# Kernel tuning notes

Hardware: AMD Instinct MI355X
Metric: run time of the kernel (lower is better)

The kernel has to match this reference:

```python
import jax, jax.numpy as jnp
import numpy as np

NUM_HEADS = 12
HEAD_DIM = 64
HIDDEN = NUM_HEADS * HEAD_DIM  # 768
B, L = 4, 512

def setup_inputs() -> dict:
    key = jax.random.key(0)
    ks = jax.random.split(key, 8)
    s = 0.02
    return {
        "hidden_states": jax.random.normal(ks[0], (B, L, HIDDEN), jnp.float32),
        "relation_embedding_k": jax.random.normal(ks[1], (B, L, L, HEAD_DIM), jnp.float32),
        "relation_embedding_v": jax.random.normal(ks[2], (B, L, L, HEAD_DIM), jnp.float32),
        "Wq": jax.random.normal(ks[3], (HIDDEN, HIDDEN), jnp.float32) * s,
        "bq": jnp.zeros((HIDDEN,), jnp.float32),
        "Wk": jax.random.normal(ks[4], (HIDDEN, HIDDEN), jnp.float32) * s,
        "bk": jnp.zeros((HIDDEN,), jnp.float32),
        "Wv": jax.random.normal(ks[5], (HIDDEN, HIDDEN), jnp.float32) * s,
        "bv": jnp.zeros((HIDDEN,), jnp.float32),
    }

def _heads(x):
    # [B, L, HIDDEN] -> [B, H, L, D]
    b, l, _ = x.shape
    return x.reshape(b, l, NUM_HEADS, HEAD_DIM).transpose(0, 2, 1, 3)

def reference(hidden_states, relation_embedding_k, relation_embedding_v,
              Wq, bq, Wk, bk, Wv, bv):
    q = _heads(hidden_states @ Wq + bq)  # [B,H,L,D]
    k = _heads(hidden_states @ Wk + bk)
    v = _heads(hidden_states @ Wv + bv)

    # content scores + relation key scores (shared across heads)
    scores = jnp.einsum('bhld,bhmd->bhlm', q, k)
    scores = scores + jnp.einsum('bhld,blrd->bhlr', q, relation_embedding_k)
    scores = scores / np.sqrt(HEAD_DIM).astype(np.float32)

    probs = jax.nn.softmax(scores, axis=-1)  # [B,H,L,L]

    ctx = jnp.einsum('bhlm,bhmd->bhld', probs, v)
    ctx = ctx + jnp.einsum('bhlr,brld->bhld', probs, relation_embedding_v)

    # [B,H,L,D] -> [B,L,HIDDEN]
    b, h, l, d = ctx.shape
    return ctx.transpose(0, 2, 1, 3).reshape(b, l, h * d)
```

## Files before the change

kernel.cpp:

```cpp
#include <hip/hip_runtime.h>
#include <stdint.h>


typedef __attribute__((ext_vector_type(8))) short bf16x8;
typedef __attribute__((ext_vector_type(4))) float f32x4;
typedef __attribute__((ext_vector_type(4))) unsigned int u32x4;

__device__ __forceinline__ unsigned short f2bf(float f) {
  union { float f; unsigned int u; } v; v.f = f;
  unsigned int r = v.u + 0x7fffu + ((v.u >> 16) & 1u);
  return (unsigned short)(r >> 16);
}
__device__ __forceinline__ float bf2f(unsigned short s) {
  union { unsigned int u; float f; } v; v.u = ((unsigned int)s) << 16;
  return v.f;
}
__device__ __forceinline__ void lds_barrier() {
  asm volatile("s_waitcnt lgkmcnt(0)\ns_barrier" ::: "memory");
}

__global__ void k_cvt_hidden(const float* __restrict__ x, unsigned short* __restrict__ y) {
  int i = blockIdx.x * 256 + threadIdx.x;
  float4 v = reinterpret_cast<const float4*>(x)[i];
  ushort4 o;
  o.x = f2bf(v.x); o.y = f2bf(v.y); o.z = f2bf(v.z); o.w = f2bf(v.w);
  reinterpret_cast<ushort4*>(y)[i] = o;
}

__global__ void k_transp_w(const float* __restrict__ Wq, const float* __restrict__ Wk,
                           const float* __restrict__ Wv, unsigned short* __restrict__ wt) {
  __shared__ float t[64][65];
  const int kt = blockIdx.x, nt = blockIdx.y, wsel = blockIdx.z;
  const float* W = wsel == 0 ? Wq : (wsel == 1 ? Wk : Wv);
  const int lx = threadIdx.x & 63, ly = threadIdx.x >> 6;
  for (int i = 0; i < 64; i += 4)
    t[ly + i][lx] = W[(size_t)(kt * 64 + ly + i) * 768 + nt * 64 + lx];
  __syncthreads();
  for (int i = 0; i < 64; i += 4) {
    int r = ly + i;
    wt[((size_t)wsel * 768 + nt * 64 + r) * 768 + kt * 64 + lx] = f2bf(t[lx][r]);
  }
}

__global__ __launch_bounds__(256) void k_qkv_gemm(
    const unsigned short* __restrict__ A, const unsigned short* __restrict__ Bt,
    const float* __restrict__ bq, const float* __restrict__ bk, const float* __restrict__ bv,
    unsigned short* __restrict__ qbf, unsigned short* __restrict__ kbf,
    unsigned short* __restrict__ vbt) {
  __shared__ __align__(16) unsigned short lA[64 * 64];
  __shared__ __align__(16) unsigned short lB[64 * 64];
  const int tid = threadIdx.x, lane = tid & 63, w = tid >> 6;
  const int m0 = blockIdx.x * 64, n0 = blockIdx.y * 64;
  const int wm = (w >> 1) * 32, wn = (w & 1) * 32;
  f32x4 acc[2][2] = {};

  for (int kt = 0; kt < 12; ++kt) {
    __syncthreads();
#pragma unroll
    for (int i = 0; i < 2; ++i) {
      int e16 = i * 256 + tid;
      int row = e16 >> 3;
      int kb = (e16 & 7) * 16;
      int dst = row * 128 + (kb ^ ((row & 7) << 4));
      u32x4 va = *(const u32x4*)((const char*)A + (size_t)(m0 + row) * 1536 + kt * 128 + kb);
      *(u32x4*)((char*)lA + dst) = va;
      u32x4 vb = *(const u32x4*)((const char*)Bt + (size_t)(n0 + row) * 1536 + kt * 128 + kb);
      *(u32x4*)((char*)lB + dst) = vb;
    }
    __syncthreads();
#pragma unroll
    for (int ks = 0; ks < 2; ++ks) {
      bf16x8 fa[2], fb[2];
      const int kbyte = (ks * 32 + (lane >> 4) * 8) * 2;
#pragma unroll
      for (int mi = 0; mi < 2; ++mi) {
        int row = wm + mi * 16 + (lane & 15);
        fa[mi] = *(const bf16x8*)((const char*)lA + row * 128 + (kbyte ^ ((row & 7) << 4)));
      }
#pragma unroll
      for (int ni = 0; ni < 2; ++ni) {
        int row = wn + ni * 16 + (lane & 15);
        fb[ni] = *(const bf16x8*)((const char*)lB + row * 128 + (kbyte ^ ((row & 7) << 4)));
      }
#pragma unroll
      for (int mi = 0; mi < 2; ++mi)
#pragma unroll
        for (int ni = 0; ni < 2; ++ni)
          acc[mi][ni] = __builtin_amdgcn_mfma_f32_16x16x32_bf16(fa[mi], fb[ni], acc[mi][ni], 0, 0, 0);
    }
  }
#pragma unroll
  for (int mi = 0; mi < 2; ++mi)
#pragma unroll
    for (int ni = 0; ni < 2; ++ni) {
      int gn = n0 + wn + ni * 16 + (lane & 15);
      float bias = (gn < 768) ? bq[gn] : (gn < 1536 ? bk[gn - 768] : bv[gn - 1536]);
#pragma unroll
      for (int r = 0; r < 4; ++r) {
        int gm = m0 + wm + mi * 16 + ((lane >> 4) << 2) + r;
        float val = acc[mi][ni][r] + bias;
        int b = gm >> 9, l = gm & 511;
        int d = gn & 63;
        if (gn < 768) {
          int h = gn >> 6;
          qbf[(((size_t)(b * 12 + h)) * 512 + l) * 64 + d] = f2bf(val);
        } else if (gn < 1536) {
          int h = (gn - 768) >> 6;
          kbf[(((size_t)(b * 12 + h)) * 512 + l) * 64 + d] = f2bf(val);
        } else {
          int h = (gn - 1536) >> 6;
          vbt[(((size_t)(b * 12 + h)) * 64 + d) * 512 + l] = f2bf(val);
        }
      }
    }
}

__global__ __launch_bounds__(256) void k_scores(
    const unsigned short* __restrict__ qbf, const unsigned short* __restrict__ kbf,
    float* __restrict__ S) {
  __shared__ __align__(16) unsigned short lQ[64 * 64];
  __shared__ __align__(16) unsigned short lK[64 * 64];
  const int tid = threadIdx.x, lane = tid & 63, w = tid >> 6;
  const int mt = blockIdx.x, lt = blockIdx.y, bh = blockIdx.z;
  const int wm = (w >> 1) * 32, wn = (w & 1) * 32;
  f32x4 acc[2][2] = {};
#pragma unroll
  for (int i = 0; i < 2; ++i) {
    int e16 = i * 256 + tid;
    int row = e16 >> 3;
    int kb = (e16 & 7) * 16;
    int dst = row * 128 + (kb ^ ((row & 7) << 4));
    u32x4 vq = *(const u32x4*)((const char*)qbf + ((size_t)bh * 512 + lt * 64 + row) * 128 + kb);
    *(u32x4*)((char*)lQ + dst) = vq;
    u32x4 vk = *(const u32x4*)((const char*)kbf + ((size_t)bh * 512 + mt * 64 + row) * 128 + kb);
    *(u32x4*)((char*)lK + dst) = vk;
  }
  __syncthreads();
#pragma unroll
  for (int ks = 0; ks < 2; ++ks) {
    bf16x8 fa[2], fb[2];
    const int kbyte = (ks * 32 + (lane >> 4) * 8) * 2;
#pragma unroll
    for (int mi = 0; mi < 2; ++mi) {
      int row = wm + mi * 16 + (lane & 15);
      fa[mi] = *(const bf16x8*)((const char*)lQ + row * 128 + (kbyte ^ ((row & 7) << 4)));
    }
#pragma unroll
    for (int ni = 0; ni < 2; ++ni) {
      int row = wn + ni * 16 + (lane & 15);
      fb[ni] = *(const bf16x8*)((const char*)lK + row * 128 + (kbyte ^ ((row & 7) << 4)));
    }
#pragma unroll
    for (int mi = 0; mi < 2; ++mi)
#pragma unroll
      for (int ni = 0; ni < 2; ++ni)
        acc[mi][ni] = __builtin_amdgcn_mfma_f32_16x16x32_bf16(fa[mi], fb[ni], acc[mi][ni], 0, 0, 0);
  }
#pragma unroll
  for (int mi = 0; mi < 2; ++mi)
#pragma unroll
    for (int ni = 0; ni < 2; ++ni) {
      int gm = mt * 64 + wn + ni * 16 + (lane & 15);
#pragma unroll
      for (int r = 0; r < 4; ++r) {
        int gl = lt * 64 + wm + mi * 16 + ((lane >> 4) << 2) + r;
        S[(size_t)bh * 262144 + (size_t)gl * 512 + gm] = acc[mi][ni][r];
      }
    }
}

__global__ __launch_bounds__(256) void k_rel(
    const unsigned short* __restrict__ qbf,
    const float* __restrict__ relk,
    const float* __restrict__ relv,
    const float* __restrict__ S,
    unsigned short* __restrict__ pbf,
    float* __restrict__ crel) {
  __shared__ __align__(16) char X[24576];
  const int tid = threadIdx.x, lane = tid & 63, w = tid >> 6;
  const int bl = blockIdx.x, b = bl >> 9, l = bl & 511;
  const int lm = lane & 15, lg = lane >> 4;

  const int hq = lm < 12 ? lm : 11;
  const char* qrow = (const char*)qbf + (((size_t)b * 12 + hq) * 512 + l) * 128;
  const bf16x8 qa0 = *(const bf16x8*)(qrow + lg * 16);
  const bf16x8 qa1 = *(const bf16x8*)(qrow + 64 + lg * 16);

  const char* rkb = (const char*)relk + (size_t)bl * 131072 +
                    (size_t)(w * 128 + lm) * 256 + lg * 32;
  f32x4 ld[3][4];
  f32x4 accA[8];
#pragma unroll
  for (int t = 0; t < 8; ++t) accA[t] = {0.f, 0.f, 0.f, 0.f};

#define LOADT(t, s)                                                  \
  {                                                                  \
    const char* p_ = rkb + (size_t)(t) * 4096;                       \
    ld[s][0] = *(const f32x4*)(p_);                                  \
    ld[s][1] = *(const f32x4*)(p_ + 16);                             \
    ld[s][2] = *(const f32x4*)(p_ + 128);                            \
    ld[s][3] = *(const f32x4*)(p_ + 144);                            \
  }
  LOADT(0, 0)
  LOADT(1, 1)
#pragma unroll
  for (int t = 0; t < 8; ++t) {
    if (t < 6) LOADT(t + 2, (t + 2) % 3)
    union { bf16x8 v; unsigned short u[8]; } fb0, fb1;
    const int s = t % 3;
#pragma unroll
    for (int j = 0; j < 4; ++j) {
      fb0.u[j] = f2bf(ld[s][0][j]);
      fb0.u[4 + j] = f2bf(ld[s][1][j]);
      fb1.u[j] = f2bf(ld[s][2][j]);
      fb1.u[4 + j] = f2bf(ld[s][3][j]);
    }
    accA[t] = __builtin_amdgcn_mfma_f32_16x16x32_bf16(qa0, fb0.v, accA[t], 0, 0, 0);
    accA[t] = __builtin_amdgcn_mfma_f32_16x16x32_bf16(qa1, fb1.v, accA[t], 0, 0, 0);
  }
#undef LOADT

  float sreg[3][8];
#pragma unroll
  for (int hh = 0; hh < 3; ++hh) {
    const float* sp = S + (((size_t)b * 12 + (w * 3 + hh)) * 512 + l) * 512 + lane;
#pragma unroll
    for (int j = 0; j < 8; ++j) sreg[hh][j] = sp[j * 64];
  }

  if (lg < 3) {
#pragma unroll
    for (int t = 0; t < 8; ++t) {
      const int r = w * 128 + t * 16 + lm;
#pragma unroll
      for (int reg = 0; reg < 4; ++reg) {
        const int h = lg * 4 + reg;
        *(float*)(X + h * 2048 + ((r * 4) ^ (lg << 6))) = accA[t][reg];
      }
    }
  }
  lds_barrier();

#pragma unroll
  for (int hh = 0; hh < 3; ++hh) {
    const int h = w * 3 + hh;
    const int sw = ((h >> 2) & 3) << 6;
    const size_t srow = (((size_t)b * 12 + h) * 512 + l) * 512;
    float sv[8];
    float mx = -1e30f;
#pragma unroll
    for (int j = 0; j < 8; ++j) {
      const int r = j * 64 + lane;
      float s = (*(const float*)(X + h * 2048 + ((r * 4) ^ sw)) + sreg[hh][j]) * 0.125f;
      sv[j] = s;
      mx = fmaxf(mx, s);
    }
#pragma unroll
    for (int off = 32; off; off >>= 1) mx = fmaxf(mx, __shfl_xor(mx, off));
    float sm = 0.f;
#pragma unroll
    for (int j = 0; j < 8; ++j) { sv[j] = __expf(sv[j] - mx); sm += sv[j]; }
#pragma unroll
    for (int off = 32; off; off >>= 1) sm += __shfl_xor(sm, off);
    const float inv = 1.f / sm;
#pragma unroll
    for (int j = 0; j < 8; ++j) {
      const int r = j * 64 + lane;
      const float pv = sv[j] * inv;
      *(float*)(X + h * 2048 + ((r * 4) ^ sw)) = pv;
      pbf[srow + r] = f2bf(pv);
    }
  }
  lds_barrier();

  float cacc[12];
#pragma unroll
  for (int h = 0; h < 12; ++h) cacc[h] = 0.f;
  const char* vptr = (const char*)relv + (size_t)b * 67108864 +
                     (size_t)(w * 128) * 131072 + (size_t)l * 256 + lane * 4;
#pragma unroll 2
  for (int rc = 0; rc < 32; ++rc) {
    const float v0 = *(const float*)(vptr);
    const float v1 = *(const float*)(vptr + 131072);
    const float v2 = *(const float*)(vptr + 262144);
    const float v3 = *(const float*)(vptr + 393216);
    vptr += 524288;
    const int r0 = w * 128 + rc * 4;
#pragma unroll
    for (int h = 0; h < 12; ++h) {
      const f32x4 p = *(const f32x4*)(X + h * 2048 + ((r0 * 4) ^ (((h >> 2) & 3) << 6)));
      cacc[h] += p[0] * v0 + p[1] * v1 + p[2] * v2 + p[3] * v3;
    }
  }
  lds_barrier();
  float* red = (float*)X;
#pragma unroll
  for (int h = 0; h < 12; ++h) red[(w * 12 + h) * 64 + lane] = cacc[h];
  lds_barrier();
  for (int i = tid; i < 768; i += 256) {
    const int h = i >> 6, d = i & 63;
    crel[(size_t)bl * 768 + i] =
        red[h * 64 + d] + red[(12 + h) * 64 + d] + red[(24 + h) * 64 + d] + red[(36 + h) * 64 + d];
  }
}

__global__ __launch_bounds__(256) void k_pv(
    const unsigned short* __restrict__ pbf, const unsigned short* __restrict__ vbt,
    const float* __restrict__ crel, float* __restrict__ out) {
  __shared__ __align__(16) unsigned short lP[64 * 64];
  __shared__ __align__(16) unsigned short lV[64 * 64];
  const int tid = threadIdx.x, lane = tid & 63, w = tid >> 6;
  const int lt = blockIdx.x, bh = blockIdx.y;
  const int b = bh / 12, h = bh % 12;
  const int wm = (w >> 1) * 32, wn = (w & 1) * 32;
  f32x4 acc[2][2] = {};
  const char* pbase = (const char*)pbf + ((size_t)bh * 512 + lt * 64) * 1024;
  const char* vbase = (const char*)vbt + (size_t)bh * 64 * 1024;
  for (int kt = 0; kt < 8; ++kt) {
    __syncthreads();
#pragma unroll
    for (int i = 0; i < 2; ++i) {
      int e16 = i * 256 + tid;
      int row = e16 >> 3;
      int kb = (e16 & 7) * 16;
      int dst = row * 128 + (kb ^ ((row & 7) << 4));
      u32x4 vp = *(const u32x4*)(pbase + (size_t)row * 1024 + kt * 128 + kb);
      *(u32x4*)((char*)lP + dst) = vp;
      u32x4 vv = *(const u32x4*)(vbase + (size_t)row * 1024 + kt * 128 + kb);
      *(u32x4*)((char*)lV + dst) = vv;
    }
    __syncthreads();
#pragma unroll
    for (int ks = 0; ks < 2; ++ks) {
      bf16x8 fa[2], fb[2];
      const int kbyte = (ks * 32 + (lane >> 4) * 8) * 2;
#pragma unroll
      for (int mi = 0; mi < 2; ++mi) {
        int row = wm + mi * 16 + (lane & 15);
        fa[mi] = *(const bf16x8*)((const char*)lP + row * 128 + (kbyte ^ ((row & 7) << 4)));
      }
#pragma unroll
      for (int ni = 0; ni < 2; ++ni) {
        int row = wn + ni * 16 + (lane & 15);
        fb[ni] = *(const bf16x8*)((const char*)lV + row * 128 + (kbyte ^ ((row & 7) << 4)));
      }
#pragma unroll
      for (int mi = 0; mi < 2; ++mi)
#pragma unroll
        for (int ni = 0; ni < 2; ++ni)
          acc[mi][ni] = __builtin_amdgcn_mfma_f32_16x16x32_bf16(fa[mi], fb[ni], acc[mi][ni], 0, 0, 0);
    }
  }
#pragma unroll
  for (int mi = 0; mi < 2; ++mi)
#pragma unroll
    for (int ni = 0; ni < 2; ++ni) {
      int gd = wn + ni * 16 + (lane & 15);
#pragma unroll
      for (int r = 0; r < 4; ++r) {
        int gl = lt * 64 + wm + mi * 16 + ((lane >> 4) << 2) + r;
        size_t o = ((size_t)b * 512 + gl) * 768 + h * 64 + gd;
        out[o] = acc[mi][ni][r] + crel[o];
      }
    }
}

extern "C" void kernel_launch(void* const* d_in, const int* in_sizes, int n_in,
                              void* d_out, int out_size, void* d_ws, size_t ws_size,
                              hipStream_t stream) {
  (void)in_sizes; (void)n_in; (void)out_size; (void)ws_size;
  const float* hidden = (const float*)d_in[0];
  const float* relk   = (const float*)d_in[1];
  const float* relv   = (const float*)d_in[2];
  const float* Wq     = (const float*)d_in[3];
  const float* bq     = (const float*)d_in[4];
  const float* Wk     = (const float*)d_in[5];
  const float* bk     = (const float*)d_in[6];
  const float* Wv     = (const float*)d_in[7];
  const float* bv     = (const float*)d_in[8];
  float* out = (float*)d_out;
  char* ws = (char*)d_ws;

  unsigned short* hb  = (unsigned short*)(ws);
  unsigned short* wt  = (unsigned short*)(ws + 3145728);
  unsigned short* qbf = (unsigned short*)(ws + 6684672);
  unsigned short* kbf = (unsigned short*)(ws + 9830400);
  unsigned short* vbt = (unsigned short*)(ws + 12976128);
  float*          S   = (float*)(ws + 16121856);
  unsigned short* pbf = (unsigned short*)(ws + 66453504);
  float*          cr  = (float*)(ws + 91619328);

  k_cvt_hidden<<<1536, 256, 0, stream>>>(hidden, hb);
  k_transp_w<<<dim3(12, 12, 3), 256, 0, stream>>>(Wq, Wk, Wv, wt);
  k_qkv_gemm<<<dim3(32, 36), 256, 0, stream>>>(hb, wt, bq, bk, bv, qbf, kbf, vbt);
  k_scores<<<dim3(8, 8, 48), 256, 0, stream>>>(qbf, kbf, S);
  k_rel<<<2048, 256, 0, stream>>>(qbf, relk, relv, S, pbf, cr);
  k_pv<<<dim3(8, 48), 256, 0, stream>>>(pbf, vbt, cr, out);
}
```

Before: 198.8 us.

## Software-pipeline relation-embedding loads in k_rel with inline asm and explicit vmcnt waits

Rewrites the memory-bound k_rel kernel so its global loads are issued through inline asm with explicit s_waitcnt vmcnt. The relk tiles and the relv rows are prefetched into triple-buffered registers, with eight relv rows per stage instead of four. The S loads are issued before the relk pipeline so they overlap, and fp32-to-bf16 conversion uses the packed v_cvt_pk_bf16_f32 instruction. The bf16 probability store is deferred until after the relv accumulation, which keeps the critical path free. This costs more live registers and uses hand-scheduled waits that depend on the exact count of outstanding loads.

```diff
diff --git a/kernel.cpp b/kernel.cpp
--- a/kernel.cpp
+++ b/kernel.cpp
@@ -18,6 +18,23 @@
 __device__ __forceinline__ void lds_barrier() {
   asm volatile("s_waitcnt lgkmcnt(0)\ns_barrier" ::: "memory");
 }
+__device__ __forceinline__ unsigned cvtpk(float lo, float hi) {
+  unsigned r;
+  asm("v_cvt_pk_bf16_f32 %0, %1, %2" : "=v"(r) : "v"(lo), "v"(hi));
+  return r;
+}
+
+#define GL16(dst, addr, OFF)                                                  \
+  asm volatile("global_load_dwordx4 %0, %1, off offset:" #OFF                \
+               : "=v"(dst) : "v"(addr))
+#define GL4(dst, addr, OFF)                                                   \
+  asm volatile("global_load_dword %0, %1, off offset:" #OFF                  \
+               : "=v"(dst) : "v"(addr))
+#define WAITV(N)                                                              \
+  do {                                                                        \
+    asm volatile("s_waitcnt vmcnt(" #N ")" ::: "memory");                     \
+    __builtin_amdgcn_sched_barrier(0);                                        \
+  } while (0)
 
 __global__ void k_cvt_hidden(const float* __restrict__ x, unsigned short* __restrict__ y) {
   int i = blockIdx.x * 256 + threadIdx.x;
@@ -180,72 +197,75 @@
   const int tid = threadIdx.x, lane = tid & 63, w = tid >> 6;
   const int bl = blockIdx.x, b = bl >> 9, l = bl & 511;
   const int lm = lane & 15, lg = lane >> 4;
-
   const int hq = lm < 12 ? lm : 11;
-  const char* qrow = (const char*)qbf + (((size_t)b * 12 + hq) * 512 + l) * 128;
-  const bf16x8 qa0 = *(const bf16x8*)(qrow + lg * 16);
-  const bf16x8 qa1 = *(const bf16x8*)(qrow + 64 + lg * 16);
-
-  const char* rkb = (const char*)relk + (size_t)bl * 131072 +
-                    (size_t)(w * 128 + lm) * 256 + lg * 32;
-  f32x4 ld[3][4];
-  f32x4 accA[8];
-#pragma unroll
-  for (int t = 0; t < 8; ++t) accA[t] = {0.f, 0.f, 0.f, 0.f};
-
-#define LOADT(t, s)                                                  \
-  {                                                                  \
-    const char* p_ = rkb + (size_t)(t) * 4096;                       \
-    ld[s][0] = *(const f32x4*)(p_);                                  \
-    ld[s][1] = *(const f32x4*)(p_ + 16);                             \
-    ld[s][2] = *(const f32x4*)(p_ + 128);                            \
-    ld[s][3] = *(const f32x4*)(p_ + 144);                            \
-  }
-  LOADT(0, 0)
-  LOADT(1, 1)
-#pragma unroll
-  for (int t = 0; t < 8; ++t) {
-    if (t < 6) LOADT(t + 2, (t + 2) % 3)
-    union { bf16x8 v; unsigned short u[8]; } fb0, fb1;
-    const int s = t % 3;
-#pragma unroll
-    for (int j = 0; j < 4; ++j) {
-      fb0.u[j] = f2bf(ld[s][0][j]);
-      fb0.u[4 + j] = f2bf(ld[s][1][j]);
-      fb1.u[j] = f2bf(ld[s][2][j]);
-      fb1.u[4 + j] = f2bf(ld[s][3][j]);
-    }
-    accA[t] = __builtin_amdgcn_mfma_f32_16x16x32_bf16(qa0, fb0.v, accA[t], 0, 0, 0);
-    accA[t] = __builtin_amdgcn_mfma_f32_16x16x32_bf16(qa1, fb1.v, accA[t], 0, 0, 0);
-  }
-#undef LOADT
+
+  union { f32x4 f; bf16x8 b; } qa0, qa1;
+  const char* aQ = (const char*)qbf + (((size_t)b * 12 + hq) * 512 + l) * 128 + (size_t)lg * 16;
+  GL16(qa0.f, aQ, 0);
+  GL16(qa1.f, aQ, 64);
 
   float sreg[3][8];
-#pragma unroll
-  for (int hh = 0; hh < 3; ++hh) {
-    const float* sp = S + (((size_t)b * 12 + (w * 3 + hh)) * 512 + l) * 512 + lane;
-#pragma unroll
-    for (int j = 0; j < 8; ++j) sreg[hh][j] = sp[j * 64];
-  }
-
-  if (lg < 3) {
-#pragma unroll
-    for (int t = 0; t < 8; ++t) {
-      const int r = w * 128 + t * 16 + lm;
-#pragma unroll
-      for (int reg = 0; reg < 4; ++reg) {
-        const int h = lg * 4 + reg;
-        *(float*)(X + h * 2048 + ((r * 4) ^ (lg << 6))) = accA[t][reg];
-      }
-    }
-  }
+  const char* aS = (const char*)S + ((((size_t)b * 12 + w * 3) * 512 + l) * 512 + lane) * 4;
+#define SRLOAD(hh)                                                            \
+  do {                                                                        \
+    const char* p_ = aS + (size_t)(hh) * 1048576;                             \
+    GL4(sreg[hh][0], p_, 0);    GL4(sreg[hh][1], p_, 256);                    \
+    GL4(sreg[hh][2], p_, 512);  GL4(sreg[hh][3], p_, 768);                    \
+    GL4(sreg[hh][4], p_, 1024); GL4(sreg[hh][5], p_, 1280);                   \
+    GL4(sreg[hh][6], p_, 1536); GL4(sreg[hh][7], p_, 1792);                   \
+  } while (0)
+  SRLOAD(0); SRLOAD(1); SRLOAD(2);
+
+  const char* aA = (const char*)relk + (size_t)bl * 131072 +
+                   (size_t)(w * 128 + lm) * 256 + (size_t)lg * 32;
+  f32x4 td[3][4];
+#define TISSUE(t, s)                                                          \
+  do {                                                                        \
+    const char* p_ = aA + (size_t)(t) * 4096;                                 \
+    GL16(td[s][0], p_, 0);   GL16(td[s][1], p_, 16);                          \
+    GL16(td[s][2], p_, 128); GL16(td[s][3], p_, 144);                         \
+  } while (0)
+  TISSUE(0, 0);
+  TISSUE(1, 1);
+
+#define ACONSUME(t, s)                                                        \
+  do {                                                                        \
+    union { bf16x8 v; unsigned u[4]; } fb0, fb1;                              \
+    fb0.u[0] = cvtpk(td[s][0][0], td[s][0][1]);                               \
+    fb0.u[1] = cvtpk(td[s][0][2], td[s][0][3]);                               \
+    fb0.u[2] = cvtpk(td[s][1][0], td[s][1][1]);                               \
+    fb0.u[3] = cvtpk(td[s][1][2], td[s][1][3]);                               \
+    fb1.u[0] = cvtpk(td[s][2][0], td[s][2][1]);                               \
+    fb1.u[1] = cvtpk(td[s][2][2], td[s][2][3]);                               \
+    fb1.u[2] = cvtpk(td[s][3][0], td[s][3][1]);                               \
+    fb1.u[3] = cvtpk(td[s][3][2], td[s][3][3]);                               \
+    f32x4 acc = {0.f, 0.f, 0.f, 0.f};                                         \
+    acc = __builtin_amdgcn_mfma_f32_16x16x32_bf16(qa0.b, fb0.v, acc, 0, 0, 0);\
+    acc = __builtin_amdgcn_mfma_f32_16x16x32_bf16(qa1.b, fb1.v, acc, 0, 0, 0);\
+    if (lg < 3) {                                                             \
+      const int r_ = w * 128 + (t) * 16 + lm;                                 \
+      _Pragma("unroll")                                                       \
+      for (int reg = 0; reg < 4; ++reg)                                       \
+        *(float*)(X + (lg * 4 + reg) * 2048 + ((r_ * 4) ^ (lg << 6))) =       \
+            acc[reg];                                                         \
+    }                                                                         \
+  } while (0)
+
+  TISSUE(2, 2); WAITV(8); ACONSUME(0, 0);
+  TISSUE(3, 0); WAITV(8); ACONSUME(1, 1);
+  TISSUE(4, 1); WAITV(8); ACONSUME(2, 2);
+  TISSUE(5, 2); WAITV(8); ACONSUME(3, 0);
+  TISSUE(6, 0); WAITV(8); ACONSUME(4, 1);
+  TISSUE(7, 1); WAITV(8); ACONSUME(5, 2);
+  WAITV(4); ACONSUME(6, 0);
+  WAITV(0); ACONSUME(7, 1);
+
   lds_barrier();
 
 #pragma unroll
   for (int hh = 0; hh < 3; ++hh) {
     const int h = w * 3 + hh;
     const int sw = ((h >> 2) & 3) << 6;
-    const size_t srow = (((size_t)b * 12 + h) * 512 + l) * 512;
     float sv[8];
     float mx = -1e30f;
 #pragma unroll
@@ -266,33 +286,82 @@
 #pragma unroll
     for (int j = 0; j < 8; ++j) {
       const int r = j * 64 + lane;
-      const float pv = sv[j] * inv;
-      *(float*)(X + h * 2048 + ((r * 4) ^ sw)) = pv;
-      pbf[srow + r] = f2bf(pv);
+      *(float*)(X + h * 2048 + ((r * 4) ^ sw)) = sv[j] * inv;
     }
   }
   lds_barrier();
 
+  const char* aV[8];
+#pragma unroll
+  for (int j = 0; j < 8; ++j)
+    aV[j] = (const char*)relv + (size_t)b * 67108864 +
+            (size_t)(w * 128 + j) * 131072 + (size_t)l * 256 + (size_t)lane * 4;
+  float vv[3][8];
+#define CISSUE(m, s)                                                          \
+  do {                                                                        \
+    GL4(vv[s][0], aV[0] + (size_t)(m) * 1048576, 0);                          \
+    GL4(vv[s][1], aV[1] + (size_t)(m) * 1048576, 0);                          \
+    GL4(vv[s][2], aV[2] + (size_t)(m) * 1048576, 0);                          \
+    GL4(vv[s][3], aV[3] + (size_t)(m) * 1048576, 0);                          \
+    GL4(vv[s][4], aV[4] + (size_t)(m) * 1048576, 0);                          \
+    GL4(vv[s][5], aV[5] + (size_t)(m) * 1048576, 0);                          \
+    GL4(vv[s][6], aV[6] + (size_t)(m) * 1048576, 0);                          \
+    GL4(vv[s][7], aV[7] + (size_t)(m) * 1048576, 0);                          \
+  } while (0)
+
   float cacc[12];
 #pragma unroll
   for (int h = 0; h < 12; ++h) cacc[h] = 0.f;
-  const char* vptr = (const char*)relv + (size_t)b * 67108864 +
-                     (size_t)(w * 128) * 131072 + (size_t)l * 256 + lane * 4;
-#pragma unroll 2
-  for (int rc = 0; rc < 32; ++rc) {
-    const float v0 = *(const float*)(vptr);
-    const float v1 = *(const float*)(vptr + 131072);
-    const float v2 = *(const float*)(vptr + 262144);
-    const float v3 = *(const float*)(vptr + 393216);
-    vptr += 524288;
-    const int r0 = w * 128 + rc * 4;
-#pragma unroll
-    for (int h = 0; h < 12; ++h) {
-      const f32x4 p = *(const f32x4*)(X + h * 2048 + ((r0 * 4) ^ (((h >> 2) & 3) << 6)));
-      cacc[h] += p[0] * v0 + p[1] * v1 + p[2] * v2 + p[3] * v3;
-    }
-  }
+
+#define CCONSUME(g, s)                                                        \
+  do {                                                                        \
+    _Pragma("unroll")                                                         \
+    for (int q = 0; q < 2; ++q) {                                             \
+      const int rb = w * 512 + (g) * 32 + q * 16;                             \
+      _Pragma("unroll")                                                       \
+      for (int h = 0; h < 12; ++h) {                                          \
+        const f32x4 p =                                                       \
+            *(const f32x4*)(X + h * 2048 + (rb ^ (((h >> 2) & 3) << 6)));     \
+        cacc[h] += p[0] * vv[s][q * 4 + 0] + p[1] * vv[s][q * 4 + 1] +        \
+                   p[2] * vv[s][q * 4 + 2] + p[3] * vv[s][q * 4 + 3];         \
+      }                                                                       \
+    }                                                                         \
+  } while (0)
+
+  CISSUE(0, 0);
+  CISSUE(1, 1);
+  CISSUE(2, 2);  WAITV(16); CCONSUME(0, 0);
+  CISSUE(3, 0);  WAITV(16); CCONSUME(1, 1);
+  CISSUE(4, 1);  WAITV(16); CCONSUME(2, 2);
+  CISSUE(5, 2);  WAITV(16); CCONSUME(3, 0);
+  CISSUE(6, 0);  WAITV(16); CCONSUME(4, 1);
+  CISSUE(7, 1);  WAITV(16); CCONSUME(5, 2);
+  CISSUE(8, 2);  WAITV(16); CCONSUME(6, 0);
+  CISSUE(9, 0);  WAITV(16); CCONSUME(7, 1);
+  CISSUE(10, 1); WAITV(16); CCONSUME(8, 2);
+  CISSUE(11, 2); WAITV(16); CCONSUME(9, 0);
+  CISSUE(12, 0); WAITV(16); CCONSUME(10, 1);
+  CISSUE(13, 1); WAITV(16); CCONSUME(11, 2);
+  CISSUE(14, 2); WAITV(16); CCONSUME(12, 0);
+  CISSUE(15, 0); WAITV(16); CCONSUME(13, 1);
+  WAITV(8);  CCONSUME(14, 2);
+  WAITV(0);  CCONSUME(15, 0);
+
   lds_barrier();
+
+#pragma unroll
+  for (int hh = 0; hh < 3; ++hh) {
+    const int h = w * 3 + hh;
+    const int sw = ((h >> 2) & 3) << 6;
+    const size_t srow = (((size_t)b * 12 + h) * 512 + l) * 512;
+#pragma unroll
+    for (int j = 0; j < 8; ++j) {
+      const int r = j * 64 + lane;
+      pbf[srow + r] = f2bf(*(const float*)(X + h * 2048 + ((r * 4) ^ sw)));
+    }
+  }
+  lds_barrier();
+
   float* red = (float*)X;
 #pragma unroll
   for (int h = 0; h < 12; ++h) red[(w * 12 + h) * 64 + lane] = cacc[h];
@@ -302,6 +371,11 @@
     crel[(size_t)bl * 768 + i] =
         red[h * 64 + d] + red[(12 + h) * 64 + d] + red[(24 + h) * 64 + d] + red[(36 + h) * 64 + d];
   }
+#undef SRLOAD
+#undef TISSUE
+#undef ACONSUME
+#undef CISSUE
+#undef CCONSUME
 }
 
 __global__ __launch_bounds__(256) void k_pv(
```

Result: faster. 194.6 us (-2.1%).
